# Kernel tuning notes

Measured on AMD Instinct MI355X. Metric: run time of the kernel, lower is better.

## Reference

```python
import jax, jax.numpy as jnp
import numpy as np

N = 8192
DIM = 64
K = 32
ALPHA = 3.0


def setup_inputs() -> dict:
    key = jax.random.key(0)
    k1, k2, k3, k4, k5, k6 = jax.random.split(key, 6)
    return {
        "idx": jnp.arange(N, dtype=jnp.int32),
        "emb1": jax.random.normal(k1, (N, DIM), dtype=jnp.float32),
        "emb2": jax.random.normal(k2, (N, DIM), dtype=jnp.float32),
        "lin1_w": jax.random.normal(k3, (DIM, DIM), dtype=jnp.float32) * (1.0 / np.sqrt(DIM)),
        "lin1_b": jax.random.normal(k4, (DIM,), dtype=jnp.float32) * 0.01,
        "lin2_w": jax.random.normal(k5, (DIM, DIM), dtype=jnp.float32) * (1.0 / np.sqrt(DIM)),
        "lin2_b": jax.random.normal(k6, (DIM,), dtype=jnp.float32) * 0.01,
    }


def reference(idx, emb1, emb2, lin1_w, lin1_b, lin2_w, lin2_b):
    n = idx.shape[0]
    nv1 = emb1[idx]                                   # [n, d]
    nv2 = emb2[idx]                                   # [n, d]
    # NOTE: source applies lin1 to BOTH branches (lin2 is unused) -- kept faithful.
    v1 = jnp.tanh(ALPHA * (nv1 @ lin1_w.T + lin1_b))  # [n, d]
    v2 = jnp.tanh(ALPHA * (nv2 @ lin1_w.T + lin1_b))  # [n, d]
    a = v1 @ v2.T - v2 @ v1.T                         # [n, n], antisymmetric
    adj = jax.nn.relu(jnp.tanh(ALPHA * a))            # [n, n]
    # per-row top-k mask; with random inputs all top-k values are > 0 a.s.,
    # so torch.nonzero keeps exactly n*K entries in row-major order.
    _, top_idx = jax.lax.top_k(adj, K)                # [n, K]
    cols = jnp.sort(top_idx, axis=1)                  # row-major (col ascending)
    rows = jnp.broadcast_to(jnp.arange(n, dtype=cols.dtype)[:, None], (n, K))
    data = jnp.take_along_axis(adj, cols, axis=1).reshape(-1)  # [n*K]
    index = jnp.stack([rows.reshape(-1), cols.reshape(-1)], axis=0)  # [2, n*K]
    return index, data
```

## Files before the change

### kernel.cpp

```cpp
#include <hip/hip_runtime.h>
#include <hip/hip_bf16.h>
#include <math.h>

#define N    8192
#define DIM  64
#define KSEL 32

__global__ __launch_bounds__(256) void embed_linear_tanh(
    const int*   __restrict__ idx,
    const float* __restrict__ emb1,
    const float* __restrict__ emb2,
    const float* __restrict__ W,
    const float* __restrict__ b,
    float* __restrict__ v1,
    float* __restrict__ v2)
{
    __shared__ float Wp[DIM][DIM + 1];
    __shared__ float e[16][DIM];

    const int t = threadIdx.x;
    const int m = blockIdx.x & 1;
    const int rowbase = (blockIdx.x >> 1) * 16;
    const float* emb  = m ? emb2 : emb1;
    float*       vout = m ? v2   : v1;

    {
        const float4* W4 = (const float4*)W;
        #pragma unroll
        for (int s = 0; s < 4; ++s) {
            int e4 = t + s * 256;
            float4 wv = W4[e4];
            int d = e4 >> 4;
            int k = (e4 & 15) * 4;
            Wp[d][k]   = wv.x; Wp[d][k+1] = wv.y;
            Wp[d][k+2] = wv.z; Wp[d][k+3] = wv.w;
        }
    }
    {
        int r = t >> 4, seg = t & 15;
        int g = idx[rowbase + r];
        float4 x = ((const float4*)(emb + (size_t)g * DIM))[seg];
        e[r][seg*4]   = x.x; e[r][seg*4+1] = x.y;
        e[r][seg*4+2] = x.z; e[r][seg*4+3] = x.w;
    }
    __syncthreads();

    const int d  = t & 63;
    const int r0 = t >> 6;
    const float bias = b[d];
    #pragma unroll
    for (int rr = 0; rr < 4; ++rr) {
        int r = r0 + rr * 4;
        float acc = bias;
        #pragma unroll
        for (int k = 0; k < DIM; ++k) acc += e[r][k] * Wp[d][k];
        vout[(size_t)(rowbase + r) * DIM + d] = tanhf(3.0f * acc);
    }
}

__global__ __launch_bounds__(256) void build_graph(
    const float* __restrict__ v1,
    const float* __restrict__ v2,
    float* __restrict__ out_rows,
    float* __restrict__ out_cols,
    float* __restrict__ out_data)
{
    __shared__ float4 c1v[16][64];
    __shared__ float4 c2v[16][64];
    __shared__ float4 vi1[4][16];
    __shared__ float4 vi2[4][16];
    __shared__ int    colbuf[4][KSEL];
    __shared__ int    wdone[4];

    const int t = threadIdx.x;
    const int w = t >> 6;
    const int l = t & 63;
    const int i = blockIdx.x * 4 + w;

    if (l < 16) {
        vi1[w][l] = ((const float4*)(v1 + (size_t)i * DIM))[l];
        vi2[w][l] = ((const float4*)(v2 + (size_t)i * DIM))[l];
    }
    if (l == 0) wdone[w] = 0;
    __syncthreads();

    int  cnt  = 0;
    bool done = false;
    const int r = t >> 2;
    const int q = t & 3;

    for (int cc = 0; cc < N / 64; ++cc) {
        const int jbase = cc * 64;
        {
            const float4* p1 = (const float4*)(v1 + (size_t)(jbase + r) * DIM) + q * 4;
            const float4* p2 = (const float4*)(v2 + (size_t)(jbase + r) * DIM) + q * 4;
            #pragma unroll
            for (int s = 0; s < 4; ++s) {
                c1v[q * 4 + s][r] = p1[s];
                c2v[q * 4 + s][r] = p2[s];
            }
        }
        __syncthreads();
        if (!done) {
            float d1 = 0.f, d2 = 0.f;
            #pragma unroll
            for (int k4 = 0; k4 < 16; ++k4) {
                float4 a1 = vi1[w][k4];
                float4 b2 = c2v[k4][l];
                d1 += a1.x * b2.x + a1.y * b2.y + a1.z * b2.z + a1.w * b2.w;
                float4 a2 = vi2[w][k4];
                float4 b1 = c1v[k4][l];
                d2 += a2.x * b1.x + a2.y * b1.y + a2.z * b1.z + a2.w * b1.w;
            }
            float a    = d1 - d2;
            float adjv = tanhf(3.0f * a);
            bool  sat  = (adjv == 1.0f);
            unsigned long long mask = __ballot(sat);
            int rank = (int)__popcll(mask & ((1ull << l) - 1ull));
            if (sat && (cnt + rank) < KSEL) colbuf[w][cnt + rank] = jbase + l;
            cnt += (int)__popcll(mask);
            if (cnt >= KSEL) { done = true; if (l == 0) wdone[w] = 1; }
        }
        __syncthreads();
        if (wdone[0] && wdone[1] && wdone[2] && wdone[3]) break;
    }

    if (cnt >= KSEL) {
        if (l < KSEL) {
            int col = colbuf[w][l];
            size_t o = (size_t)i * KSEL + l;
            out_rows[o] = (float)i;
            out_cols[o] = (float)col;
            out_data[o] = 1.0f;
        }
    } else if (l == 0) {
        float bv[KSEL]; int bc[KSEL];
        #pragma unroll
        for (int k = 0; k < KSEL; ++k) { bv[k] = -1.0f; bc[k] = 0; }
        for (int j = 0; j < N; ++j) {
            float d1 = 0.f, d2 = 0.f;
            for (int k = 0; k < DIM; ++k) {
                d1 += v1[(size_t)i * DIM + k] * v2[(size_t)j * DIM + k];
                d2 += v2[(size_t)i * DIM + k] * v1[(size_t)j * DIM + k];
            }
            float adjv = fmaxf(tanhf(3.0f * (d1 - d2)), 0.0f);
            if (adjv > bv[KSEL - 1]) {
                int p = KSEL - 1;
                while (p > 0 && bv[p - 1] < adjv) {
                    bv[p] = bv[p - 1]; bc[p] = bc[p - 1]; --p;
                }
                bv[p] = adjv; bc[p] = j;
            }
        }
        for (int x = 1; x < KSEL; ++x) {
            float tv = bv[x]; int tc = bc[x]; int y = x - 1;
            while (y >= 0 && bc[y] > tc) { bv[y+1] = bv[y]; bc[y+1] = bc[y]; --y; }
            bv[y + 1] = tv; bc[y + 1] = tc;
        }
        for (int k = 0; k < KSEL; ++k) {
            size_t o = (size_t)i * KSEL + k;
            out_rows[o] = (float)i;
            out_cols[o] = (float)bc[k];
            out_data[o] = bv[k];
        }
    }
}

extern "C" void kernel_launch(void* const* d_in, const int* in_sizes, int n_in,
                              void* d_out, int out_size, void* d_ws, size_t ws_size,
                              hipStream_t stream) {
    const int*   idx  = (const int*)  d_in[0];
    const float* emb1 = (const float*)d_in[1];
    const float* emb2 = (const float*)d_in[2];
    const float* w1   = (const float*)d_in[3];
    const float* b1   = (const float*)d_in[4];

    float* v1 = (float*)d_ws;
    float* v2 = v1 + (size_t)N * DIM;

    float* out      = (float*)d_out;
    float* out_rows = out;
    float* out_cols = out + (size_t)N * KSEL;
    float* out_data = out + (size_t)2 * N * KSEL;

    embed_linear_tanh<<<2 * N / 16, 256, 0, stream>>>(idx, emb1, emb2, w1, b1, v1, v2);
    build_graph<<<N / 4, 256, 0, stream>>>(v1, v2, out_rows, out_cols, out_data);
}
```

Measured before the change: 98.83 us.

## Process four rows per wave to reuse each column tile across rows

build_graph now assigns 16 rows per block (4 per wavefront) instead of 4. Each lane loads its column's v1/v2 vectors from shared memory into registers once per tile and reuses them for all four rows, with per-row saturation counters and early exit once every row has 32 hits. This cuts global and LDS traffic per row by about 4x. The cost is a quarter as many blocks, more register pressure from the 128-float register tile, and each block running until its slowest row finishes.

Measured after the change: 93.46 us. 1.06x faster.

```diff
diff --git a/kernel.cpp b/kernel.cpp
--- a/kernel.cpp
+++ b/kernel.cpp
@@ -58,7 +58,7 @@
     }
 }
 
-__global__ __launch_bounds__(256) void build_graph(
+__global__ __launch_bounds__(256, 2) void build_graph(
     const float* __restrict__ v1,
     const float* __restrict__ v2,
     float* __restrict__ out_rows,
@@ -67,24 +67,25 @@
 {
     __shared__ float4 c1v[16][64];
     __shared__ float4 c2v[16][64];
-    __shared__ float4 vi1[4][16];
-    __shared__ float4 vi2[4][16];
-    __shared__ int    colbuf[4][KSEL];
+    __shared__ float4 vi1[16][16];
+    __shared__ float4 vi2[16][16];
+    __shared__ int    colbuf[16][KSEL];
     __shared__ int    wdone[4];
 
     const int t = threadIdx.x;
     const int w = t >> 6;
     const int l = t & 63;
-    const int i = blockIdx.x * 4 + w;
-
-    if (l < 16) {
-        vi1[w][l] = ((const float4*)(v1 + (size_t)i * DIM))[l];
-        vi2[w][l] = ((const float4*)(v2 + (size_t)i * DIM))[l];
+    const int rowbase = blockIdx.x * 16;
+
+    {
+        int r = t >> 4, seg = t & 15;
+        vi1[r][seg] = ((const float4*)(v1 + (size_t)(rowbase + r) * DIM))[seg];
+        vi2[r][seg] = ((const float4*)(v2 + (size_t)(rowbase + r) * DIM))[seg];
     }
     if (l == 0) wdone[w] = 0;
     __syncthreads();
 
-    int  cnt  = 0;
+    int  cnt[4] = {0, 0, 0, 0};
     bool done = false;
     const int r = t >> 2;
     const int q = t & 3;
@@ -101,67 +102,85 @@
             }
         }
         __syncthreads();
+
         if (!done) {
-            float d1 = 0.f, d2 = 0.f;
-            #pragma unroll
-            for (int k4 = 0; k4 < 16; ++k4) {
-                float4 a1 = vi1[w][k4];
-                float4 b2 = c2v[k4][l];
-                d1 += a1.x * b2.x + a1.y * b2.y + a1.z * b2.z + a1.w * b2.w;
-                float4 a2 = vi2[w][k4];
-                float4 b1 = c1v[k4][l];
-                d2 += a2.x * b1.x + a2.y * b1.y + a2.z * b1.z + a2.w * b1.w;
-            }
-            float a    = d1 - d2;
-            float adjv = tanhf(3.0f * a);
-            bool  sat  = (adjv == 1.0f);
-            unsigned long long mask = __ballot(sat);
-            int rank = (int)__popcll(mask & ((1ull << l) - 1ull));
-            if (sat && (cnt + rank) < KSEL) colbuf[w][cnt + rank] = jbase + l;
-            cnt += (int)__popcll(mask);
-            if (cnt >= KSEL) { done = true; if (l == 0) wdone[w] = 1; }
+            float4 c1r[16], c2r[16];
+            #pragma unroll
+            for (int k4 = 0; k4 < 16; ++k4) { c1r[k4] = c1v[k4][l]; c2r[k4] = c2v[k4][l]; }
+
+            bool all_done = true;
+            #pragma unroll
+            for (int rr = 0; rr < 4; ++rr) {
+                if (cnt[rr] < KSEL) {
+                    const int wrow = w * 4 + rr;
+                    float d1 = 0.f, d2 = 0.f;
+                    #pragma unroll
+                    for (int k4 = 0; k4 < 16; ++k4) {
+                        float4 a1 = vi1[wrow][k4];
+                        float4 b2 = c2r[k4];
+                        d1 += a1.x * b2.x + a1.y * b2.y + a1.z * b2.z + a1.w * b2.w;
+                        float4 a2 = vi2[wrow][k4];
+                        float4 b1 = c1r[k4];
+                        d2 += a2.x * b1.x + a2.y * b1.y + a2.z * b1.z + a2.w * b1.w;
+                    }
+                    float a    = d1 - d2;
+                    float adjv = tanhf(3.0f * a);
+                    bool  sat  = (adjv == 1.0f);
+                    unsigned long long mask = __ballot(sat);
+                    int rank = (int)__popcll(mask & ((1ull << l) - 1ull));
+                    if (sat && (cnt[rr] + rank) < KSEL) colbuf[wrow][cnt[rr] + rank] = jbase + l;
+                    cnt[rr] += (int)__popcll(mask);
+                    if (cnt[rr] < KSEL) all_done = false;
+                }
+            }
+            if (all_done) { done = true; if (l == 0) wdone[w] = 1; }
         }
         __syncthreads();
         if (wdone[0] && wdone[1] && wdone[2] && wdone[3]) break;
     }
 
-    if (cnt >= KSEL) {
-        if (l < KSEL) {
-            int col = colbuf[w][l];
-            size_t o = (size_t)i * KSEL + l;
-            out_rows[o] = (float)i;
-            out_cols[o] = (float)col;
-            out_data[o] = 1.0f;
-        }
-    } else if (l == 0) {
-        float bv[KSEL]; int bc[KSEL];
-        #pragma unroll
-        for (int k = 0; k < KSEL; ++k) { bv[k] = -1.0f; bc[k] = 0; }
-        for (int j = 0; j < N; ++j) {
-            float d1 = 0.f, d2 = 0.f;
-            for (int k = 0; k < DIM; ++k) {
-                d1 += v1[(size_t)i * DIM + k] * v2[(size_t)j * DIM + k];
-                d2 += v2[(size_t)i * DIM + k] * v1[(size_t)j * DIM + k];
-            }
-            float adjv = fmaxf(tanhf(3.0f * (d1 - d2)), 0.0f);
-            if (adjv > bv[KSEL - 1]) {
-                int p = KSEL - 1;
-                while (p > 0 && bv[p - 1] < adjv) {
-                    bv[p] = bv[p - 1]; bc[p] = bc[p - 1]; --p;
+    #pragma unroll
+    for (int rr = 0; rr < 4; ++rr) {
+        const int wrow = w * 4 + rr;
+        const int i = rowbase + wrow;
+        if (cnt[rr] >= KSEL) {
+            if (l < KSEL) {
+                int col = colbuf[wrow][l];
+                size_t o = (size_t)i * KSEL + l;
+                out_rows[o] = (float)i;
+                out_cols[o] = (float)col;
+                out_data[o] = 1.0f;
+            }
+        } else if (l == 0) {
+            float bv[KSEL]; int bc[KSEL];
+            #pragma unroll
+            for (int k = 0; k < KSEL; ++k) { bv[k] = -1.0f; bc[k] = 0; }
+            for (int j = 0; j < N; ++j) {
+                float d1 = 0.f, d2 = 0.f;
+                for (int k = 0; k < DIM; ++k) {
+                    d1 += v1[(size_t)i * DIM + k] * v2[(size_t)j * DIM + k];
+                    d2 += v2[(size_t)i * DIM + k] * v1[(size_t)j * DIM + k];
                 }
-                bv[p] = adjv; bc[p] = j;
-            }
-        }
-        for (int x = 1; x < KSEL; ++x) {
-            float tv = bv[x]; int tc = bc[x]; int y = x - 1;
-            while (y >= 0 && bc[y] > tc) { bv[y+1] = bv[y]; bc[y+1] = bc[y]; --y; }
-            bv[y + 1] = tv; bc[y + 1] = tc;
-        }
-        for (int k = 0; k < KSEL; ++k) {
-            size_t o = (size_t)i * KSEL + k;
-            out_rows[o] = (float)i;
-            out_cols[o] = (float)bc[k];
-            out_data[o] = bv[k];
+                float adjv = fmaxf(tanhf(3.0f * (d1 - d2)), 0.0f);
+                if (adjv > bv[KSEL - 1]) {
+                    int p = KSEL - 1;
+                    while (p > 0 && bv[p - 1] < adjv) {
+                        bv[p] = bv[p - 1]; bc[p] = bc[p - 1]; --p;
+                    }
+                    bv[p] = adjv; bc[p] = j;
+                }
+            }
+            for (int x = 1; x < KSEL; ++x) {
+                float tv = bv[x]; int tc = bc[x]; int y = x - 1;
+                while (y >= 0 && bc[y] > tc) { bv[y+1] = bv[y]; bc[y+1] = bc[y]; --y; }
+                bv[y + 1] = tv; bc[y + 1] = tc;
+            }
+            for (int k = 0; k < KSEL; ++k) {
+                size_t o = (size_t)i * KSEL + k;
+                out_rows[o] = (float)i;
+                out_cols[o] = (float)bc[k];
+                out_data[o] = bv[k];
+            }
         }
     }
 }
@@ -184,5 +203,5 @@
     float* out_data = out + (size_t)2 * N * KSEL;
 
     embed_linear_tanh<<<2 * N / 16, 256, 0, stream>>>(idx, emb1, emb2, w1, b1, v1, v2);
-    build_graph<<<N / 4, 256, 0, stream>>>(v1, v2, out_rows, out_cols, out_data);
+    build_graph<<<N / 16, 256, 0, stream>>>(v1, v2, out_rows, out_cols, out_data);
 }
```
